# Kernel tuning notes

Hardware: AMD Instinct MI355X
Metric: run time of the kernel (lower is better)

## Reference

```python
import jax, jax.numpy as jnp
import numpy as np

R_MAX = 6.0        # BesselBasis r_max (apax default scale)
NUM_RADIAL = 16    # BesselBasis num basis functions
MAX_Z = 119        # chemical embedding vocab
NUM_FEATURES = 128


def _sph_deg3(u):
    """Real spherical harmonics (Racah normalization, Y_00=1) of unit vectors u [E,3],
    degrees 0..3 -> 16 components, m ordered -l..l per degree."""
    x, y, z = u[..., 0], u[..., 1], u[..., 2]
    s3, s15, s10_4, s6_4, s15_2 = jnp.sqrt(3.0), jnp.sqrt(15.0), jnp.sqrt(10.0) / 4, jnp.sqrt(6.0) / 4, jnp.sqrt(15.0) / 2
    x2, y2, z2 = x * x, y * y, z * z
    return jnp.stack([
        jnp.ones_like(x),                     # l=0
        y, z, x,                              # l=1
        s3 * x * y, s3 * y * z, 0.5 * (3 * z2 - 1.0), s3 * x * z, 0.5 * s3 * (x2 - y2),  # l=2
        s10_4 * y * (3 * x2 - y2), s15 * x * y * z, s6_4 * y * (5 * z2 - 1.0),
        0.5 * z * (5 * z2 - 3.0), s6_4 * x * (5 * z2 - 1.0), s15_2 * z * (x2 - y2),
        s10_4 * x * (x2 - 3 * y2),            # l=3
    ], axis=-1)


def setup_inputs() -> dict:
    key = jax.random.key(0)
    k1, k2, k3, k4 = jax.random.split(key, 4)
    E, N = 1_600_000, 50_000
    dr_vec = jax.random.normal(k1, (E, 3), jnp.float32)
    Z = jax.random.randint(k2, (N,), 0, MAX_Z, jnp.int32)
    idx = jax.random.randint(k3, (2, E), 0, N, jnp.int32)
    emb_table = jax.random.normal(k4, (MAX_Z, NUM_FEATURES), jnp.float32) * 0.02
    return {"dr_vec": dr_vec, "Z": Z, "idx": idx, "emb_table": emb_table}


def reference(dr_vec, Z, idx, emb_table):
    N = Z.shape[0]
    i, j = idx[0], idx[1]
    pair_mask = (i != j).astype(dr_vec.dtype)            # [E]
    node_mask = (Z != 0).astype(dr_vec.dtype)            # [N]

    # chemical embedding (gather), masked
    scalar_features = emb_table[Z] * node_mask[:, None]  # [N,F]

    # distances, cosine cutoff, masking
    r = jnp.linalg.norm(dr_vec, axis=-1)                 # [E]
    cutoffs = 0.5 * (jnp.cos(jnp.pi * r / R_MAX) + 1.0) * (r < R_MAX).astype(dr_vec.dtype)
    cutoffs = cutoffs * pair_mask

    # neighborhood size per node, scattered back to edges
    nbh = jax.ops.segment_sum(cutoffs, i, num_segments=N)[i]      # [E]
    pair_scale = jnp.where(pair_mask > 0, 1.0 / jnp.where(nbh > 0, nbh, 1.0), 0.0)

    # Bessel radial basis: sqrt(2/rmax) * sin(n*pi*r/rmax)/r, n=1..NUM_RADIAL
    n = jnp.arange(1, NUM_RADIAL + 1, dtype=dr_vec.dtype)
    safe_r = jnp.where(r > 1e-12, r, 1e-12)[:, None]
    radial_expansion = jnp.sqrt(2.0 / R_MAX) * jnp.sin(n * jnp.pi * safe_r / R_MAX) / safe_r
    radial_expansion = radial_expansion * cutoffs[:, None]        # [E,16]

    # spherical harmonics of unit displacement, scaled, scatter-aggregated
    u = dr_vec / safe_r
    spherical_expansion = _sph_deg3(u) * pair_scale[:, None]      # [E,16]
    spherical_features = jax.ops.segment_sum(spherical_expansion, i, num_segments=N)
    spherical_features = spherical_features * node_mask[:, None]  # [N,16]

    # aggregate radial expansion too so the full gather-compute-scatter chain is live
    radial_features = jax.ops.segment_sum(radial_expansion, i, num_segments=N) * node_mask[:, None]

    # num_layers=0: return all produced node features concatenated [N, 128+16+16]
    return jnp.concatenate([scalar_features, spherical_features, radial_features], axis=-1)
```

## Files before the change

### kernel.cpp

```cpp
#include <hip/hip_runtime.h>

#define P1_T 1024
#define P1_E 8
#define P1_SPAN (P1_T * P1_E)
#define NBK_MAX 800
#define CCAP 2560
#define P2_T 256
#define P2_C ((CCAP + P2_T - 1) / P2_T)

typedef unsigned long long u64;

__device__ __forceinline__ u64 pack19(float x, float y, float z, int li) {
    int xq = min(max((int)rintf(x * 32768.0f) + 262144, 0), 524287);
    int yq = min(max((int)rintf(y * 32768.0f) + 262144, 0), 524287);
    int zq = min(max(((int)rintf(z * 32768.0f)) + 262144, 0), 524287);
    return ((u64)li << 57) | ((u64)zq << 38) | ((u64)yq << 19) | (u64)xq;
}

__global__ void k_bin8(const int* __restrict__ idx, const float* __restrict__ dr,
                       int* __restrict__ ccnt, u64* __restrict__ bucket,
                       int E, int nbk) {
    __shared__ u64 s_pld[P1_SPAN];
    __shared__ int s_hist[NBK_MAX];
    __shared__ int s_off[NBK_MAX + 1];
    __shared__ int s_cur[NBK_MAX];
    __shared__ int s_gd[NBK_MAX];
    __shared__ int s_wt[16];

    int tid = threadIdx.x, wave = tid >> 6, lane = tid & 63;
    for (int b = tid; b < nbk; b += P1_T) { s_hist[b] = 0; s_cur[b] = 0; }
    if (tid < 16) s_wt[tid] = 0;

    long long e0 = (long long)blockIdx.x * P1_SPAN + (long long)tid * P1_E;
    bool full = (e0 + P1_E <= E);

    int iv[P1_E], jv[P1_E];
    float f[3 * P1_E];
    if (full) {
        int4 a = *(const int4*)(idx + e0);
        int4 b = *(const int4*)(idx + e0 + 4);
        iv[0] = a.x; iv[1] = a.y; iv[2] = a.z; iv[3] = a.w;
        iv[4] = b.x; iv[5] = b.y; iv[6] = b.z; iv[7] = b.w;
        int4 c = *(const int4*)(idx + E + e0);
        int4 d = *(const int4*)(idx + E + e0 + 4);
        jv[0] = c.x; jv[1] = c.y; jv[2] = c.z; jv[3] = c.w;
        jv[4] = d.x; jv[5] = d.y; jv[6] = d.z; jv[7] = d.w;
        const float4* dp = (const float4*)(dr + 3 * e0);
#pragma unroll
        for (int q = 0; q < 6; q++) {
            float4 v = dp[q];
            f[4 * q + 0] = v.x; f[4 * q + 1] = v.y;
            f[4 * q + 2] = v.z; f[4 * q + 3] = v.w;
        }
    } else {
#pragma unroll
        for (int k = 0; k < P1_E; k++) {
            long long e = e0 + k;
            if (e < E) {
                iv[k] = idx[e]; jv[k] = idx[E + e];
                f[3 * k + 0] = dr[3 * e + 0];
                f[3 * k + 1] = dr[3 * e + 1];
                f[3 * k + 2] = dr[3 * e + 2];
            } else { iv[k] = -1; jv[k] = 0; }
        }
    }
    __syncthreads();

#pragma unroll
    for (int k = 0; k < P1_E; k++)
        if (iv[k] >= 0 && iv[k] != jv[k]) atomicAdd(&s_hist[iv[k] >> 6], 1);
    __syncthreads();

    int nw = (nbk + 63) >> 6;
    if (wave < nw) {
        int i0 = wave * 64 + lane;
        int h = (i0 < nbk) ? s_hist[i0] : 0;
        int v = h;
#pragma unroll
        for (int d = 1; d < 64; d <<= 1) {
            int u = __shfl_up(v, d);
            if (lane >= d) v += u;
        }
        if (lane == 63) s_wt[wave] = v;
        if (i0 < nbk) s_off[i0] = v - h;
    }
    __syncthreads();
    if (tid == 0) {
        int run = 0;
#pragma unroll
        for (int w = 0; w < 16; w++) { int t = s_wt[w]; s_wt[w] = run; run += t; }
        s_off[nbk] = run;
    }
    __syncthreads();
    if (wave < nw) {
        int i0 = wave * 64 + lane;
        if (i0 < nbk) s_off[i0] += s_wt[wave];
    }
    __syncthreads();

    for (int b = tid; b < nbk; b += P1_T) {
        int h = s_hist[b];
        int gb = (h > 0) ? atomicAdd(&ccnt[b], h) : 0;
        s_gd[b] = gb - s_off[b];
    }

#pragma unroll
    for (int k = 0; k < P1_E; k++) {
        if (iv[k] >= 0 && iv[k] != jv[k]) {
            int b = iv[k] >> 6;
            int pos = s_off[b] + atomicAdd(&s_cur[b], 1);
            s_pld[pos] = pack19(f[3 * k + 0], f[3 * k + 1], f[3 * k + 2], iv[k] & 63);
        }
    }
    __syncthreads();

    int total = s_off[nbk];
    int p0 = tid * P1_E;
    if (p0 < total) {
        int lo = 0, hi = nbk;
        while (hi - lo > 1) {
            int mid = (lo + hi) >> 1;
            if (s_off[mid] <= p0) lo = mid; else hi = mid;
        }
        int b = lo;
        int pe = min(p0 + P1_E, total);
        for (int p = p0; p < pe; p++) {
            while (p >= s_off[b + 1]) b++;
            int lidx = s_gd[b] + p;
            if (lidx < CCAP) bucket[(long long)b * CCAP + lidx] = s_pld[p];
        }
    }
}

__global__ void k_node7(const int* __restrict__ Z,
                        const int* __restrict__ ccnt,
                        const u64* __restrict__ bucket,
                        const float* __restrict__ emb,
                        float* __restrict__ out, int N) {
    __shared__ u64 s_sorted[CCAP];
    __shared__ int s_hist[4][64];
    __shared__ int s_cur[4][64];
    __shared__ int s_start[64];
    __shared__ int s_deg[64];

    int g = blockIdx.x;
    int tid = threadIdx.x;
    int wave = tid >> 6;
    int node0 = g << 6;
    int cnt = ccnt[g];
    if (cnt > CCAP) cnt = CCAP;
    const u64* bk = bucket + (long long)g * CCAP;

    s_hist[wave][tid & 63] = 0;

    u64 pld[P2_C];
    int pli[P2_C];
#pragma unroll
    for (int c = 0; c < P2_C; c++) {
        int t = tid + c * P2_T;
        pli[c] = 64;
        if (t < cnt) { pld[c] = bk[t]; pli[c] = (int)(pld[c] >> 57); }
    }

#pragma unroll
    for (int c = 0; c < 8; c++) {
        int t = tid + c * P2_T;
        int li = t >> 5, q = t & 31;
        int n = node0 + li;
        if (n < N) {
            int zn = Z[n];
            float4 v = make_float4(0.f, 0.f, 0.f, 0.f);
            if (zn != 0) v = ((const float4*)emb)[(long long)zn * 32 + q];
            ((float4*)out)[(long long)n * 40 + q] = v;
        }
    }

#pragma unroll
    for (int c = 0; c < P2_C; c++)
        if (pli[c] < 64) atomicAdd(&s_hist[wave][pli[c]], 1);
    __syncthreads();

    if (tid < 64) {
        int h0 = s_hist[0][tid], h1 = s_hist[1][tid];
        int h2 = s_hist[2][tid], h3 = s_hist[3][tid];
        int tot = h0 + h1 + h2 + h3;
        int v = tot;
#pragma unroll
        for (int d = 1; d < 64; d <<= 1) {
            int u = __shfl_up(v, d);
            if (tid >= d) v += u;
        }
        int st = v - tot;
        s_start[tid] = st;
        s_deg[tid] = tot;
        s_cur[0][tid] = st;
        s_cur[1][tid] = st + h0;
        s_cur[2][tid] = st + h0 + h1;
        s_cur[3][tid] = st + h0 + h1 + h2;
    }
    __syncthreads();

#pragma unroll
    for (int c = 0; c < P2_C; c++) {
        if (pli[c] < 64) {
            int pos = atomicAdd(&s_cur[wave][pli[c]], 1);
            s_sorted[pos] = pld[c];
        }
    }
    __syncthreads();

    const float s3   = 1.7320508075688772f;
    const float s15  = 3.872983346207417f;
    const float s104 = 0.7905694150420949f;
    const float s64c = 0.6123724356957945f;
    const float s152 = 1.936491673103709f;
    const float inv_scale = 3.0517578125e-05f;

    int lane = tid & 63;
    int group = lane >> 3;
    int sub = lane & 7;

    for (int round = 0; round < 2; round++) {
        int li = (round << 5) + (wave << 3) + group;
        int n = node0 + li;
        int st = s_start[li];
        int deg = s_deg[li];

        float acc[33];
#pragma unroll
        for (int k = 0; k < 33; k++) acc[k] = 0.0f;

        for (int p = sub; p < deg; p += 8) {
            u64 v = s_sorted[st + p];
            float x = (float)((int)(v & 524287) - 262144) * inv_scale;
            float y = (float)((int)((v >> 19) & 524287) - 262144) * inv_scale;
            float z = (float)((int)((v >> 38) & 524287) - 262144) * inv_scale;
            float r = sqrtf(x * x + y * y + z * z);
            float rs = fmaxf(r, 1e-12f);
            float inv_r = 1.0f / rs;
            float s, c;
            __sincosf(0.5235987755982988f * rs, &s, &c);
            float cut = (r < 6.0f) ? (0.5f * (c + 1.0f)) : 0.0f;
            acc[32] += cut;

            float ux = x * inv_r, uy = y * inv_r, uz = z * inv_r;
            float x2 = ux * ux, y2 = uy * uy, z2 = uz * uz;

            acc[0] += 1.0f;
            acc[1] += uy;
            acc[2] += uz;
            acc[3] += ux;
            acc[4] += s3 * ux * uy;
            acc[5] += s3 * uy * uz;
            acc[6] += 0.5f * (3.0f * z2 - 1.0f);
            acc[7] += s3 * ux * uz;
            acc[8] += 0.5f * s3 * (x2 - y2);
            acc[9] += s104 * uy * (3.0f * x2 - y2);
            acc[10] += s15 * ux * uy * uz;
            acc[11] += s64c * uy * (5.0f * z2 - 1.0f);
            acc[12] += 0.5f * uz * (5.0f * z2 - 3.0f);
            acc[13] += s64c * ux * (5.0f * z2 - 1.0f);
            acc[14] += s152 * uz * (x2 - y2);
            acc[15] += s104 * ux * (x2 - 3.0f * y2);

            float coef = 0.5773502691896258f * inv_r * cut;
            float twoc = 2.0f * c;
            float sp = 0.0f, sn = s;
#pragma unroll
            for (int nn = 0; nn < 16; nn++) {
                acc[16 + nn] += coef * sn;
                float nx = twoc * sn - sp;
                sp = sn; sn = nx;
            }
        }

#pragma unroll
        for (int k = 0; k < 33; k++) {
            float v = acc[k];
            v += __shfl_xor(v, 4);
            v += __shfl_xor(v, 2);
            v += __shfl_xor(v, 1);
            acc[k] = v;
        }

        if (sub == 0 && n < N) {
            float zmask = (Z[n] != 0) ? 1.0f : 0.0f;
            float nbh = acc[32];
            float ps = (nbh > 0.0f) ? (1.0f / nbh) : 1.0f;
            float sphs = ps * zmask;
            float4* o4 = (float4*)(out + (long long)n * 160);
#pragma unroll
            for (int q = 0; q < 4; q++) {
                o4[32 + q] = make_float4(acc[4 * q] * sphs, acc[4 * q + 1] * sphs,
                                         acc[4 * q + 2] * sphs, acc[4 * q + 3] * sphs);
            }
#pragma unroll
            for (int q = 0; q < 4; q++) {
                o4[36 + q] = make_float4(acc[16 + 4 * q] * zmask, acc[17 + 4 * q] * zmask,
                                         acc[18 + 4 * q] * zmask, acc[19 + 4 * q] * zmask);
            }
        }
    }
}

extern "C" void kernel_launch(void* const* d_in, const int* in_sizes, int n_in,
                              void* d_out, int out_size, void* d_ws, size_t ws_size,
                              hipStream_t stream) {
    const float* dr = (const float*)d_in[0];
    const int* Z = (const int*)d_in[1];
    const int* idx = (const int*)d_in[2];
    const float* emb = (const float*)d_in[3];
    float* out = (float*)d_out;

    int E = in_sizes[0] / 3;
    int N = in_sizes[1];
    int nbk = (N + 63) >> 6;

    int* ccnt = (int*)d_ws;
    u64* bucket = (u64*)(ccnt + ((NBK_MAX + 1) & ~1));

    hipMemsetAsync(ccnt, 0, (size_t)NBK_MAX * sizeof(int), stream);

    int g1 = (E + P1_SPAN - 1) / P1_SPAN;
    k_bin8<<<g1, P1_T, 0, stream>>>(idx, dr, ccnt, bucket, E, nbk);

    k_node7<<<nbk, P2_T, 0, stream>>>(Z, ccnt, bucket, emb, out, N);
}
```

Measured before the change: 124.0 us.

## Move embedding gather to bin kernel, use one node per group with wider blocks

Shrinks the binning block to 512 threads and loops the per-chunk prefix scan over waves so each wave can handle several chunks. The embedding gather and output write move into the binning kernel as a grid-stride loop. The node kernel goes to 512 threads so each 8-lane group handles one node in a single round. It also prefetches the next packed edge and computes the Bessel sines with a shallower double-angle recurrence. The aim is to shorten the critical path of the node kernel and spread the embedding copy over more blocks, at the cost of more shared-memory histograms and a larger binning grid.

After: 123.4 us. Within noise of the previous version (-0.5%).

```diff
diff --git a/kernel.cpp b/kernel.cpp
--- a/kernel.cpp
+++ b/kernel.cpp
@@ -1,11 +1,11 @@
 #include <hip/hip_runtime.h>
 
-#define P1_T 1024
+#define P1_T 512
 #define P1_E 8
 #define P1_SPAN (P1_T * P1_E)
 #define NBK_MAX 800
 #define CCAP 2560
-#define P2_T 256
+#define P2_T 512
 #define P2_C ((CCAP + P2_T - 1) / P2_T)
 
 typedef unsigned long long u64;
@@ -18,8 +18,10 @@
 }
 
 __global__ void k_bin8(const int* __restrict__ idx, const float* __restrict__ dr,
+                       const int* __restrict__ Z, const float* __restrict__ emb,
+                       float* __restrict__ out,
                        int* __restrict__ ccnt, u64* __restrict__ bucket,
-                       int E, int nbk) {
+                       int E, int N, int nbk) {
     __shared__ u64 s_pld[P1_SPAN];
     __shared__ int s_hist[NBK_MAX];
     __shared__ int s_off[NBK_MAX + 1];
@@ -71,9 +73,9 @@
         if (iv[k] >= 0 && iv[k] != jv[k]) atomicAdd(&s_hist[iv[k] >> 6], 1);
     __syncthreads();
 
-    int nw = (nbk + 63) >> 6;
-    if (wave < nw) {
-        int i0 = wave * 64 + lane;
+    int nchunk = (nbk + 63) >> 6;
+    for (int ch = wave; ch < nchunk; ch += (P1_T >> 6)) {
+        int i0 = ch * 64 + lane;
         int h = (i0 < nbk) ? s_hist[i0] : 0;
         int v = h;
 #pragma unroll
@@ -81,7 +83,7 @@
             int u = __shfl_up(v, d);
             if (lane >= d) v += u;
         }
-        if (lane == 63) s_wt[wave] = v;
+        if (lane == 63) s_wt[ch] = v;
         if (i0 < nbk) s_off[i0] = v - h;
     }
     __syncthreads();
@@ -92,9 +94,9 @@
         s_off[nbk] = run;
     }
     __syncthreads();
-    if (wave < nw) {
-        int i0 = wave * 64 + lane;
-        if (i0 < nbk) s_off[i0] += s_wt[wave];
+    for (int ch = wave; ch < nchunk; ch += (P1_T >> 6)) {
+        int i0 = ch * 64 + lane;
+        if (i0 < nbk) s_off[i0] += s_wt[ch];
     }
     __syncthreads();
 
@@ -130,28 +132,37 @@
             if (lidx < CCAP) bucket[(long long)b * CCAP + lidx] = s_pld[p];
         }
     }
+
+    long long TQ = (long long)gridDim.x * P1_T;
+    for (long long t = (long long)blockIdx.x * P1_T + tid; t < (long long)N * 32; t += TQ) {
+        int n = (int)(t >> 5), q = (int)(t & 31);
+        int zn = Z[n];
+        float4 v = make_float4(0.f, 0.f, 0.f, 0.f);
+        if (zn != 0) v = ((const float4*)emb)[(long long)zn * 32 + q];
+        ((float4*)out)[(long long)n * 40 + q] = v;
+    }
 }
 
-__global__ void k_node7(const int* __restrict__ Z,
+__global__ void k_node8(const int* __restrict__ Z,
                         const int* __restrict__ ccnt,
                         const u64* __restrict__ bucket,
-                        const float* __restrict__ emb,
                         float* __restrict__ out, int N) {
     __shared__ u64 s_sorted[CCAP];
-    __shared__ int s_hist[4][64];
-    __shared__ int s_cur[4][64];
+    __shared__ int s_hist[8][64];
+    __shared__ int s_cur[8][64];
     __shared__ int s_start[64];
     __shared__ int s_deg[64];
 
     int g = blockIdx.x;
     int tid = threadIdx.x;
     int wave = tid >> 6;
+    int lane = tid & 63;
     int node0 = g << 6;
     int cnt = ccnt[g];
     if (cnt > CCAP) cnt = CCAP;
     const u64* bk = bucket + (long long)g * CCAP;
 
-    s_hist[wave][tid & 63] = 0;
+    ((int*)s_hist)[tid] = 0;
 
     u64 pld[P2_C];
     int pli[P2_C];
@@ -163,27 +174,14 @@
     }
 
 #pragma unroll
-    for (int c = 0; c < 8; c++) {
-        int t = tid + c * P2_T;
-        int li = t >> 5, q = t & 31;
-        int n = node0 + li;
-        if (n < N) {
-            int zn = Z[n];
-            float4 v = make_float4(0.f, 0.f, 0.f, 0.f);
-            if (zn != 0) v = ((const float4*)emb)[(long long)zn * 32 + q];
-            ((float4*)out)[(long long)n * 40 + q] = v;
-        }
-    }
-
-#pragma unroll
     for (int c = 0; c < P2_C; c++)
         if (pli[c] < 64) atomicAdd(&s_hist[wave][pli[c]], 1);
     __syncthreads();
 
     if (tid < 64) {
-        int h0 = s_hist[0][tid], h1 = s_hist[1][tid];
-        int h2 = s_hist[2][tid], h3 = s_hist[3][tid];
-        int tot = h0 + h1 + h2 + h3;
+        int h[8], tot = 0;
+#pragma unroll
+        for (int w = 0; w < 8; w++) { h[w] = s_hist[w][tid]; tot += h[w]; }
         int v = tot;
 #pragma unroll
         for (int d = 1; d < 64; d <<= 1) {
@@ -193,10 +191,9 @@
         int st = v - tot;
         s_start[tid] = st;
         s_deg[tid] = tot;
-        s_cur[0][tid] = st;
-        s_cur[1][tid] = st + h0;
-        s_cur[2][tid] = st + h0 + h1;
-        s_cur[3][tid] = st + h0 + h1 + h2;
+        int run = st;
+#pragma unroll
+        for (int w = 0; w < 8; w++) { s_cur[w][tid] = run; run += h[w]; }
     }
     __syncthreads();
 
@@ -216,89 +213,110 @@
     const float s152 = 1.936491673103709f;
     const float inv_scale = 3.0517578125e-05f;
 
-    int lane = tid & 63;
     int group = lane >> 3;
     int sub = lane & 7;
-
-    for (int round = 0; round < 2; round++) {
-        int li = (round << 5) + (wave << 3) + group;
-        int n = node0 + li;
-        int st = s_start[li];
-        int deg = s_deg[li];
-
-        float acc[33];
-#pragma unroll
-        for (int k = 0; k < 33; k++) acc[k] = 0.0f;
-
-        for (int p = sub; p < deg; p += 8) {
-            u64 v = s_sorted[st + p];
-            float x = (float)((int)(v & 524287) - 262144) * inv_scale;
-            float y = (float)((int)((v >> 19) & 524287) - 262144) * inv_scale;
-            float z = (float)((int)((v >> 38) & 524287) - 262144) * inv_scale;
-            float r = sqrtf(x * x + y * y + z * z);
-            float rs = fmaxf(r, 1e-12f);
-            float inv_r = 1.0f / rs;
-            float s, c;
-            __sincosf(0.5235987755982988f * rs, &s, &c);
-            float cut = (r < 6.0f) ? (0.5f * (c + 1.0f)) : 0.0f;
-            acc[32] += cut;
-
-            float ux = x * inv_r, uy = y * inv_r, uz = z * inv_r;
-            float x2 = ux * ux, y2 = uy * uy, z2 = uz * uz;
-
-            acc[0] += 1.0f;
-            acc[1] += uy;
-            acc[2] += uz;
-            acc[3] += ux;
-            acc[4] += s3 * ux * uy;
-            acc[5] += s3 * uy * uz;
-            acc[6] += 0.5f * (3.0f * z2 - 1.0f);
-            acc[7] += s3 * ux * uz;
-            acc[8] += 0.5f * s3 * (x2 - y2);
-            acc[9] += s104 * uy * (3.0f * x2 - y2);
-            acc[10] += s15 * ux * uy * uz;
-            acc[11] += s64c * uy * (5.0f * z2 - 1.0f);
-            acc[12] += 0.5f * uz * (5.0f * z2 - 3.0f);
-            acc[13] += s64c * ux * (5.0f * z2 - 1.0f);
-            acc[14] += s152 * uz * (x2 - y2);
-            acc[15] += s104 * ux * (x2 - 3.0f * y2);
-
-            float coef = 0.5773502691896258f * inv_r * cut;
-            float twoc = 2.0f * c;
-            float sp = 0.0f, sn = s;
-#pragma unroll
-            for (int nn = 0; nn < 16; nn++) {
-                acc[16 + nn] += coef * sn;
-                float nx = twoc * sn - sp;
-                sp = sn; sn = nx;
-            }
-        }
-
-#pragma unroll
-        for (int k = 0; k < 33; k++) {
-            float v = acc[k];
-            v += __shfl_xor(v, 4);
-            v += __shfl_xor(v, 2);
-            v += __shfl_xor(v, 1);
-            acc[k] = v;
-        }
-
-        if (sub == 0 && n < N) {
-            float zmask = (Z[n] != 0) ? 1.0f : 0.0f;
-            float nbh = acc[32];
-            float ps = (nbh > 0.0f) ? (1.0f / nbh) : 1.0f;
-            float sphs = ps * zmask;
-            float4* o4 = (float4*)(out + (long long)n * 160);
-#pragma unroll
-            for (int q = 0; q < 4; q++) {
-                o4[32 + q] = make_float4(acc[4 * q] * sphs, acc[4 * q + 1] * sphs,
-                                         acc[4 * q + 2] * sphs, acc[4 * q + 3] * sphs);
-            }
-#pragma unroll
-            for (int q = 0; q < 4; q++) {
-                o4[36 + q] = make_float4(acc[16 + 4 * q] * zmask, acc[17 + 4 * q] * zmask,
-                                         acc[18 + 4 * q] * zmask, acc[19 + 4 * q] * zmask);
-            }
+    int li = (wave << 3) + group;
+    int n = node0 + li;
+    int st = s_start[li];
+    int deg = s_deg[li];
+
+    float acc[33];
+#pragma unroll
+    for (int k = 0; k < 33; k++) acc[k] = 0.0f;
+
+    int p = sub;
+    u64 v = (p < deg) ? s_sorted[st + p] : 0ULL;
+    while (p < deg) {
+        int pn = p + 8;
+        u64 vn = (pn < deg) ? s_sorted[st + pn] : 0ULL;
+
+        float x = (float)((int)(v & 524287) - 262144) * inv_scale;
+        float y = (float)((int)((v >> 19) & 524287) - 262144) * inv_scale;
+        float z = (float)((int)((v >> 38) & 524287) - 262144) * inv_scale;
+        float r = sqrtf(x * x + y * y + z * z);
+        float rs = fmaxf(r, 1e-12f);
+        float inv_r = 1.0f / rs;
+        float s, c;
+        __sincosf(0.5235987755982988f * rs, &s, &c);
+        float cut = (r < 6.0f) ? (0.5f * (c + 1.0f)) : 0.0f;
+        acc[32] += cut;
+
+        float ux = x * inv_r, uy = y * inv_r, uz = z * inv_r;
+        float x2 = ux * ux, y2 = uy * uy, z2 = uz * uz;
+
+        acc[0] += 1.0f;
+        acc[1] += uy;
+        acc[2] += uz;
+        acc[3] += ux;
+        acc[4] += s3 * ux * uy;
+        acc[5] += s3 * uy * uz;
+        acc[6] += 0.5f * (3.0f * z2 - 1.0f);
+        acc[7] += s3 * ux * uz;
+        acc[8] += 0.5f * s3 * (x2 - y2);
+        acc[9] += s104 * uy * (3.0f * x2 - y2);
+        acc[10] += s15 * ux * uy * uz;
+        acc[11] += s64c * uy * (5.0f * z2 - 1.0f);
+        acc[12] += 0.5f * uz * (5.0f * z2 - 3.0f);
+        acc[13] += s64c * ux * (5.0f * z2 - 1.0f);
+        acc[14] += s152 * uz * (x2 - y2);
+        acc[15] += s104 * ux * (x2 - 3.0f * y2);
+
+        float coef = 0.5773502691896258f * inv_r * cut;
+        float s1 = s, c1 = c;
+        float s2 = 2.0f * s1 * c1;
+        float c2 = 2.0f * c1 * c1 - 1.0f;
+        float sn3 = s2 * c1 + c2 * s1;
+        float s4 = 2.0f * s2 * c2;
+        float c4 = 2.0f * c2 * c2 - 1.0f;
+        float t4 = 2.0f * c4;
+        float s5  = t4 * s1 + sn3;
+        float s6  = t4 * s2 + s2;
+        float s7  = t4 * sn3 + s1;
+        float s8  = t4 * s4;
+        float s9  = t4 * s5 - s1;
+        float s10v = t4 * s6 - s2;
+        float s11 = t4 * s7 - sn3;
+        float s12 = t4 * s8 - s4;
+        float s13 = t4 * s9 - s5;
+        float s14 = t4 * s10v - s6;
+        float s15v = t4 * s11 - s7;
+        float s16 = t4 * s12 - s8;
+        acc[16] += coef * s1;   acc[17] += coef * s2;
+        acc[18] += coef * sn3;  acc[19] += coef * s4;
+        acc[20] += coef * s5;   acc[21] += coef * s6;
+        acc[22] += coef * s7;   acc[23] += coef * s8;
+        acc[24] += coef * s9;   acc[25] += coef * s10v;
+        acc[26] += coef * s11;  acc[27] += coef * s12;
+        acc[28] += coef * s13;  acc[29] += coef * s14;
+        acc[30] += coef * s15v; acc[31] += coef * s16;
+
+        p = pn; v = vn;
+    }
+
+#pragma unroll
+    for (int k = 0; k < 33; k++) {
+        float vv = acc[k];
+        vv += __shfl_xor(vv, 4);
+        vv += __shfl_xor(vv, 2);
+        vv += __shfl_xor(vv, 1);
+        acc[k] = vv;
+    }
+
+    if (sub == 0 && n < N) {
+        float zmask = (Z[n] != 0) ? 1.0f : 0.0f;
+        float nbh = acc[32];
+        float ps = (nbh > 0.0f) ? (1.0f / nbh) : 1.0f;
+        float sphs = ps * zmask;
+        float4* o4 = (float4*)(out + (long long)n * 160);
+#pragma unroll
+        for (int q = 0; q < 4; q++) {
+            o4[32 + q] = make_float4(acc[4 * q] * sphs, acc[4 * q + 1] * sphs,
+                                     acc[4 * q + 2] * sphs, acc[4 * q + 3] * sphs);
+        }
+#pragma unroll
+        for (int q = 0; q < 4; q++) {
+            o4[36 + q] = make_float4(acc[16 + 4 * q] * zmask, acc[17 + 4 * q] * zmask,
+                                     acc[18 + 4 * q] * zmask, acc[19 + 4 * q] * zmask);
         }
     }
 }
@@ -322,7 +340,7 @@
     hipMemsetAsync(ccnt, 0, (size_t)NBK_MAX * sizeof(int), stream);
 
     int g1 = (E + P1_SPAN - 1) / P1_SPAN;
-    k_bin8<<<g1, P1_T, 0, stream>>>(idx, dr, ccnt, bucket, E, nbk);
-
-    k_node7<<<nbk, P2_T, 0, stream>>>(Z, ccnt, bucket, emb, out, N);
+    k_bin8<<<g1, P1_T, 0, stream>>>(idx, dr, Z, emb, out, ccnt, bucket, E, N, nbk);
+
+    k_node8<<<nbk, P2_T, 0, stream>>>(Z, ccnt, bucket, out, N);
 }
```
